# Performance work log

Hardware: AMD Instinct MI355X
Metric: run time of the kernel (lower is better)

Reference implementation:

```python
import jax, jax.numpy as jnp
import numpy as np
import math

B, LQ, LK = 4, 1024, 2048
QD, KD, VD = 768, 512, 512
H, NH = 1024, 16
HD = H // NH

def setup_inputs() -> dict:
    key = jax.random.key(0)
    ks = jax.random.split(key, 11)
    s = 0.02
    return {
        "query": jax.random.normal(ks[0], (B, LQ, QD), jnp.float32),
        "key": jax.random.normal(ks[1], (B, LK, KD), jnp.float32),
        "value": jax.random.normal(ks[2], (B, LK, VD), jnp.float32),
        "Wq": jax.random.normal(ks[3], (QD, H), jnp.float32) * s,
        "bq": jnp.zeros((H,), jnp.float32),
        "Wk": jax.random.normal(ks[4], (KD, H), jnp.float32) * s,
        "bk": jnp.zeros((H,), jnp.float32),
        "Wv": jax.random.normal(ks[5], (VD, H), jnp.float32) * s,
        "bv": jnp.zeros((H,), jnp.float32),
        "Wo": jax.random.normal(ks[6], (H, H), jnp.float32) * s,
        "bo": jnp.zeros((H,), jnp.float32),
    }

def reference(query, key, value, Wq, bq, Wk, bk, Wv, bv, Wo, bo):
    # project and split heads: [B, L, H] -> [B, NH, L, HD]
    def heads(x):
        b, l, _ = x.shape
        return x.reshape(b, l, NH, HD).transpose(0, 2, 1, 3)
    q = heads(query @ Wq + bq)   # [B, NH, LQ, HD]
    k = heads(key @ Wk + bk)     # [B, NH, LK, HD]
    v = heads(value @ Wv + bv)   # [B, NH, LK, HD]
    scores = jnp.einsum('bhqd,bhkd->bhqk', q, k) / math.sqrt(HD)
    weights = jax.nn.softmax(scores, axis=-1)  # dropout inactive (eval / rate used deterministically as identity)
    att = jnp.einsum('bhqk,bhkd->bhqd', weights, v)
    att = att.transpose(0, 2, 1, 3).reshape(query.shape[0], -1, H)
    out = att @ Wo + bo
    return out
```

## Files before the change

### kernel.cpp

```cpp
#include <hip/hip_runtime.h>
#include <math.h>

using bf16x8 = __attribute__((ext_vector_type(8))) short;
using f32x4  = __attribute__((ext_vector_type(4))) float;
using u32x2  = __attribute__((ext_vector_type(2))) unsigned int;

namespace {
constexpr int kB  = 4;
constexpr int kLQ = 1024;
constexpr int kLK = 2048;
constexpr int kH  = 1024;
constexpr int kHD = 64;
}

__device__ __forceinline__ unsigned short f2bf(float x) {
  union { float f; unsigned int u; } v; v.f = x;
  unsigned int r = v.u + 0x7fffu + ((v.u >> 16) & 1u);
  return (unsigned short)(r >> 16);
}

typedef const __attribute__((address_space(1))) unsigned int guint_t;
typedef __attribute__((address_space(3))) unsigned int luint_t;
__device__ __forceinline__ void g2l16(const void* g, void* l) {
  __builtin_amdgcn_global_load_lds(
      (guint_t*)g,
      (luint_t*)(unsigned int)(unsigned long long)l,
      16, 0, 0);
}

__global__ __launch_bounds__(256) void prep_kernel(
    const float* __restrict__ q, const float* __restrict__ k,
    const float* __restrict__ v, const float* __restrict__ Wq,
    const float* __restrict__ Wk, const float* __restrict__ Wv,
    const float* __restrict__ Wo, unsigned short* __restrict__ qo,
    unsigned short* __restrict__ ko, unsigned short* __restrict__ vo,
    unsigned short* __restrict__ WqT, unsigned short* __restrict__ WkT,
    unsigned short* __restrict__ WvT, unsigned short* __restrict__ WoT)
{
  __shared__ float tile[64][65];
  const int t = threadIdx.x;
  if (blockIdx.x < 5632) {
    int c = blockIdx.x * 256 + t;
    const float* src; unsigned short* dst;
    if (c < 393216)      { src = q; dst = qo; }
    else if (c < 917504) { src = k; dst = ko; c -= 393216; }
    else                 { src = v; dst = vo; c -= 917504; }
    const int i = c * 8;
    const float4 a = *(const float4*)(src + i);
    const float4 b = *(const float4*)(src + i + 4);
    uint4 o;
    o.x = (unsigned int)f2bf(a.x) | ((unsigned int)f2bf(a.y) << 16);
    o.y = (unsigned int)f2bf(a.z) | ((unsigned int)f2bf(a.w) << 16);
    o.z = (unsigned int)f2bf(b.x) | ((unsigned int)f2bf(b.y) << 16);
    o.w = (unsigned int)f2bf(b.z) | ((unsigned int)f2bf(b.w) << 16);
    *(uint4*)(dst + i) = o;
    return;
  }
  int id = blockIdx.x - 5632;
  const float* W; unsigned short* Wt; int Kd;
  if (id < 192)      { W = Wq; Wt = WqT; Kd = 768; }
  else if (id < 320) { W = Wk; Wt = WkT; Kd = 512;  id -= 192; }
  else if (id < 448) { W = Wv; Wt = WvT; Kd = 512;  id -= 320; }
  else               { W = Wo; Wt = WoT; Kd = 1024; id -= 448; }
  const int Nd = 1024;
  const int n0 = (id & 15) * 64;
  const int k0 = (id >> 4) * 64;
  const int rr = t >> 4;
  const int c4 = t & 15;
#pragma unroll
  for (int i = 0; i < 4; ++i) {
    const int row = i * 16 + rr;
    const float4 vv = *(const float4*)(W + (size_t)(k0 + row) * Nd + n0 + c4 * 4);
    tile[row][c4*4+0] = vv.x; tile[row][c4*4+1] = vv.y;
    tile[row][c4*4+2] = vv.z; tile[row][c4*4+3] = vv.w;
  }
  __syncthreads();
#pragma unroll
  for (int i = 0; i < 4; ++i) {
    const int n = i * 16 + rr;
    ushort4 o;
    o.x = f2bf(tile[c4*4+0][n]); o.y = f2bf(tile[c4*4+1][n]);
    o.z = f2bf(tile[c4*4+2][n]); o.w = f2bf(tile[c4*4+3][n]);
    *(ushort4*)(Wt + (size_t)(n0 + n) * Kd + k0 + c4 * 4) = o;
  }
}

__device__ __forceinline__ void gemm_body(
    const unsigned short* __restrict__ A, const unsigned short* __restrict__ Bt,
    const float* __restrict__ bias, void* __restrict__ Cout,
    int N, int K, int bx, int by, int mode, float scale, char* lds)
{
  const int t    = threadIdx.x;
  const int lane = t & 63;
  const int w    = t >> 6;
  const int l15  = lane & 15;
  const int lq8  = (lane >> 4) * 8;
  const int lq4  = (lane >> 4) * 4;
  const int r0   = by * 128;
  const int c0   = bx * 128;
  const int wm   = w >> 1, wn = w & 1;

  f32x4 acc[4][4] = {};

  const unsigned short* gsrc[4];
  char* ldst[4];
#pragma unroll
  for (int i = 0; i < 4; ++i) {
    const int g = w * 4 + i;
    const unsigned short* src = (g < 8) ? A : Bt;
    const int rbase = (g < 8) ? (r0 + g * 16) : (c0 + (g - 8) * 16);
    gsrc[i] = src + (size_t)(rbase + l15) * K + lq8;
    ldst[i] = lds + g * 1024 + lane * 16;
  }

#pragma unroll
  for (int i = 0; i < 4; ++i) g2l16(gsrc[i], ldst[i]);
#pragma unroll
  for (int i = 0; i < 4; ++i) g2l16(gsrc[i] + 32, ldst[i] + 16384);

  int slot = 0;
  for (int k0 = 0; k0 < K; k0 += 32) {
    if (k0 + 32 < K) {
      asm volatile("s_waitcnt vmcnt(4)\n\ts_barrier" ::: "memory");
    } else {
      asm volatile("s_waitcnt vmcnt(0)\n\ts_barrier" ::: "memory");
    }
    char* buf = lds + slot * 16384;
    if (k0 + 64 < K) {
      int ns = slot + 2; if (ns >= 3) ns -= 3;
#pragma unroll
      for (int i = 0; i < 4; ++i)
        g2l16(gsrc[i] + k0 + 64, ldst[i] + ns * 16384);
    }
    bf16x8 af[4], bfr[4];
#pragma unroll
    for (int i = 0; i < 4; ++i) af[i]  = *(const bf16x8*)(buf + (wm*4 + i) * 1024 + lane * 16);
#pragma unroll
    for (int j = 0; j < 4; ++j) bfr[j] = *(const bf16x8*)(buf + 8192 + (wn*4 + j) * 1024 + lane * 16);
#pragma unroll
    for (int i = 0; i < 4; ++i)
#pragma unroll
      for (int j = 0; j < 4; ++j)
        acc[i][j] = (mode == 2)
          ? __builtin_amdgcn_mfma_f32_16x16x32_bf16(af[i], bfr[j], acc[i][j], 0, 0, 0)
          : __builtin_amdgcn_mfma_f32_16x16x32_bf16(bfr[j], af[i], acc[i][j], 0, 0, 0);
    slot = (slot == 2) ? 0 : slot + 1;
  }

  if (mode == 2) {
#pragma unroll
    for (int j = 0; j < 4; ++j) {
      const int col = c0 + wn * 64 + j * 16 + l15;
      const float bcol = bias[col];
#pragma unroll
      for (int i = 0; i < 4; ++i) {
        const int row = r0 + wm * 64 + i * 16 + lq4;
        unsigned short* out = (unsigned short*)Cout;
        const int bb = row >> 11;
        const int lk = row & 2047;
        ushort4 o;
        o.x = f2bf(acc[i][j][0] + bcol); o.y = f2bf(acc[i][j][1] + bcol);
        o.z = f2bf(acc[i][j][2] + bcol); o.w = f2bf(acc[i][j][3] + bcol);
        *(ushort4*)(out + (size_t)(bb * kH + col) * kLK + lk) = o;
      }
    }
  } else {
#pragma unroll
    for (int i = 0; i < 4; ++i) {
      const int row = r0 + wm * 64 + i * 16 + l15;
#pragma unroll
      for (int j = 0; j < 4; ++j) {
        const int ncol = c0 + wn * 64 + j * 16 + lq4;
        const float4 b4 = *(const float4*)(bias + ncol);
        if (mode == 0) {
          float4 o;
          o.x = acc[i][j][0] + b4.x; o.y = acc[i][j][1] + b4.y;
          o.z = acc[i][j][2] + b4.z; o.w = acc[i][j][3] + b4.w;
          *(float4*)((float*)Cout + (size_t)row * N + ncol) = o;
        } else {
          ushort4 o;
          o.x = f2bf((acc[i][j][0] + b4.x) * scale);
          o.y = f2bf((acc[i][j][1] + b4.y) * scale);
          o.z = f2bf((acc[i][j][2] + b4.z) * scale);
          o.w = f2bf((acc[i][j][3] + b4.w) * scale);
          *(ushort4*)((unsigned short*)Cout + (size_t)row * N + ncol) = o;
        }
      }
    }
  }
}

__global__ __launch_bounds__(256) void qkv_gemm_kernel(
    const unsigned short* __restrict__ qA, const unsigned short* __restrict__ WqT,
    const float* __restrict__ bq, unsigned short* __restrict__ Qb,
    const unsigned short* __restrict__ kA, const unsigned short* __restrict__ WkT,
    const float* __restrict__ bk, unsigned short* __restrict__ Kb,
    const unsigned short* __restrict__ vA, const unsigned short* __restrict__ WvT,
    const float* __restrict__ bv, unsigned short* __restrict__ Vtw)
{
  __shared__ __align__(16) char lds[49152];
  int id = blockIdx.x;
  if (id < 256) {
    gemm_body(qA, WqT, bq, Qb, 1024, 768, id & 7, id >> 3, 1,
              0.18033688011112042f, lds);
  } else if (id < 768) {
    id -= 256;
    gemm_body(kA, WkT, bk, Kb, 1024, 512, id & 7, id >> 3, 1, 1.f, lds);
  } else {
    id -= 768;
    gemm_body(vA, WvT, bv, Vtw, 1024, 512, id & 7, id >> 3, 2, 1.f, lds);
  }
}

__global__ __launch_bounds__(256) void out_gemm_kernel(
    const unsigned short* __restrict__ A, const unsigned short* __restrict__ Bt,
    const float* __restrict__ bias, float* __restrict__ C)
{
  __shared__ __align__(16) char lds[49152];
  const int id = blockIdx.x;
  gemm_body(A, Bt, bias, C, 1024, 1024, id & 7, id >> 3, 0, 1.f, lds);
}

__global__ __launch_bounds__(512) void attn_mfma_kernel(
    const unsigned short* __restrict__ Q, const unsigned short* __restrict__ K,
    const unsigned short* __restrict__ Vt, unsigned short* __restrict__ O)
{
  __shared__ __align__(16) char lds[49152];
  constexpr int POFF = 32768;
  const int t    = threadIdx.x;
  const int lane = t & 63;
  const int w    = t >> 6;
  const int l15  = lane & 15;
  const int lg   = lane >> 4;
  const int lq8  = lg * 8;
  const int lq4  = lg * 4;
  const int flat = blockIdx.x;
  const int bh   = flat & 63;
  const int qb   = flat >> 6;
  const int h    = bh & 15;
  const int b    = bh >> 4;
  const int q0   = qb * 128;
  const int hoff = h * kHD;
  constexpr int NT = kLK / 64;

  bf16x8 qf[2];
#pragma unroll
  for (int kh = 0; kh < 2; ++kh)
    qf[kh] = *(const bf16x8*)(Q + (size_t)(b*kLQ + q0 + w*16 + l15) * kH
                                + hoff + kh*32 + lq8);

  f32x4 acc[4] = {};
  float lsum = 0.f;

  const int swz  = ((l15 * 5) & 7) << 4;
  const int colw = (lg * 8)  ^ swz;
  const int colr = (lg * 16) ^ swz;
  char* const prow = lds + POFF + (w*16 + l15) * 128;

  const unsigned short* gsrc[2];
  int gstep[2];
  char* ldst[2];
#pragma unroll
  for (int i = 0; i < 2; ++i) {
    const int g = w * 2 + i;
    if (g < 8) {
      gsrc[i]  = K + (size_t)(b*kLK + (g >> 1)*16 + l15) * kH + hoff + (g & 1)*32 + lq8;
      gstep[i] = 64 * kH;
    } else {
      const int gg = g - 8;
      gsrc[i]  = Vt + (size_t)(b*kH + hoff + (gg >> 1)*16 + l15) * kLK + (gg & 1)*32 + lq8;
      gstep[i] = 64;
    }
    ldst[i] = lds + g * 1024 + lane * 16;
  }

  g2l16(gsrc[0], ldst[0]);
  g2l16(gsrc[1], ldst[1]);

  for (int kt = 0; kt < NT; ++kt) {
    asm volatile("s_waitcnt vmcnt(0)\n\ts_barrier" ::: "memory");
    char* buf = lds + (kt & 1) * 16384;
    if (kt + 1 < NT) {
      const int ns = (kt + 1) & 1;
      g2l16(gsrc[0] + (size_t)(kt + 1) * gstep[0], ldst[0] + ns * 16384);
      g2l16(gsrc[1] + (size_t)(kt + 1) * gstep[1], ldst[1] + ns * 16384);
    }

    f32x4 s[4];
#pragma unroll
    for (int kcf = 0; kcf < 4; ++kcf) {
      const bf16x8 kf0 = *(const bf16x8*)(buf + (kcf*2 + 0) * 1024 + lane * 16);
      const bf16x8 kf1 = *(const bf16x8*)(buf + (kcf*2 + 1) * 1024 + lane * 16);
      f32x4 z = {};
      z = __builtin_amdgcn_mfma_f32_16x16x32_bf16(kf0, qf[0], z, 0, 0, 0);
      z = __builtin_amdgcn_mfma_f32_16x16x32_bf16(kf1, qf[1], z, 0, 0, 0);
      s[kcf] = z;
    }

#pragma unroll
    for (int kcf = 0; kcf < 4; ++kcf) {
      const float p0 = __builtin_amdgcn_exp2f(s[kcf][0]);
      const float p1 = __builtin_amdgcn_exp2f(s[kcf][1]);
      const float p2 = __builtin_amdgcn_exp2f(s[kcf][2]);
      const float p3 = __builtin_amdgcn_exp2f(s[kcf][3]);
      lsum += (p0 + p1) + (p2 + p3);
      u32x2 pw;
      pw.x = __builtin_amdgcn_perm(__float_as_uint(p1), __float_as_uint(p0), 0x07060302u);
      pw.y = __builtin_amdgcn_perm(__float_as_uint(p3), __float_as_uint(p2), 0x07060302u);
      *(u32x2*)(prow + (colw ^ (kcf * 32))) = pw;
    }

    bf16x8 pf[2];
#pragma unroll
    for (int kq = 0; kq < 2; ++kq)
      pf[kq] = *(const bf16x8*)(prow + (colr ^ (kq * 64)));
#pragma unroll
    for (int vd = 0; vd < 4; ++vd) {
      const bf16x8 vf0 = *(const bf16x8*)(buf + 8192 + (vd*2 + 0) * 1024 + lane * 16);
      const bf16x8 vf1 = *(const bf16x8*)(buf + 8192 + (vd*2 + 1) * 1024 + lane * 16);
      acc[vd] = __builtin_amdgcn_mfma_f32_16x16x32_bf16(vf0, pf[0], acc[vd], 0, 0, 0);
      acc[vd] = __builtin_amdgcn_mfma_f32_16x16x32_bf16(vf1, pf[1], acc[vd], 0, 0, 0);
    }
  }

  float v = lsum;
  v += __shfl_xor(v, 16);
  v += __shfl_xor(v, 32);
  const float rinv = 1.f / v;
#pragma unroll
  for (int vd = 0; vd < 4; ++vd) {
    ushort4 o;
    o.x = f2bf(acc[vd][0] * rinv);
    o.y = f2bf(acc[vd][1] * rinv);
    o.z = f2bf(acc[vd][2] * rinv);
    o.w = f2bf(acc[vd][3] * rinv);
    *(ushort4*)(O + (size_t)(b*kLQ + q0 + w*16 + l15) * kH
                  + hoff + vd*16 + lq4) = o;
  }
}

extern "C" void kernel_launch(void* const* d_in, const int* in_sizes, int n_in,
                              void* d_out, int out_size, void* d_ws, size_t ws_size,
                              hipStream_t stream) {
  (void)in_sizes; (void)n_in; (void)out_size; (void)ws_size;
  const float* query = (const float*)d_in[0];
  const float* key   = (const float*)d_in[1];
  const float* value = (const float*)d_in[2];
  const float* Wq = (const float*)d_in[3];
  const float* bq = (const float*)d_in[4];
  const float* Wk = (const float*)d_in[5];
  const float* bk = (const float*)d_in[6];
  const float* Wv = (const float*)d_in[7];
  const float* bv = (const float*)d_in[8];
  const float* Wo = (const float*)d_in[9];
  const float* bo = (const float*)d_in[10];
  float* out = (float*)d_out;

  unsigned short* ws  = (unsigned short*)d_ws;
  unsigned short* qA  = ws;
  unsigned short* kA  = qA  + 3145728;
  unsigned short* vA  = kA  + 4194304;
  unsigned short* WqT = vA  + 4194304;
  unsigned short* WkT = WqT + 786432;
  unsigned short* WvT = WkT + 524288;
  unsigned short* WoT = WvT + 524288;
  unsigned short* Qb  = WoT + 1048576;
  unsigned short* Kb  = Qb  + 4194304;
  unsigned short* Vtw = Kb  + 8388608;
  unsigned short* Ab  = Vtw + 8388608;

  prep_kernel<<<6336, 256, 0, stream>>>(query, key, value, Wq, Wk, Wv, Wo,
                                        qA, kA, vA, WqT, WkT, WvT, WoT);
  qkv_gemm_kernel<<<1280, 256, 0, stream>>>(qA, WqT, bq, Qb,
                                            kA, WkT, bk, Kb,
                                            vA, WvT, bv, Vtw);
  attn_mfma_kernel<<<512, 512, 0, stream>>>(Qb, Kb, Vtw, Ab);
  out_gemm_kernel<<<256, 256, 0, stream>>>(Ab, WoT, bo, out);
}
```

Before: 225.4 us.

## Load GEMM B operand directly from global into registers, stage only A in LDS

The projection GEMMs now stage only the A tile in LDS through the triple-buffered async path. Each wave loads its B fragments straight from global memory into registers and prefetches the next k-step's fragments during the MFMAs. LDS usage per block drops by half, which could raise occupancy and cut LDS traffic. The cost is that B is no longer shared through LDS, so global loads for B are duplicated across the two wm waves. The vmcnt waits are also retuned to account for the register loads, and B-load latency may not be fully hidden.

```diff
diff --git a/kernel.cpp b/kernel.cpp
--- a/kernel.cpp
+++ b/kernel.cpp
@@ -102,48 +102,58 @@
 
   f32x4 acc[4][4] = {};
 
-  const unsigned short* gsrc[4];
-  char* ldst[4];
-#pragma unroll
-  for (int i = 0; i < 4; ++i) {
-    const int g = w * 4 + i;
-    const unsigned short* src = (g < 8) ? A : Bt;
-    const int rbase = (g < 8) ? (r0 + g * 16) : (c0 + (g - 8) * 16);
-    gsrc[i] = src + (size_t)(rbase + l15) * K + lq8;
-    ldst[i] = lds + g * 1024 + lane * 16;
-  }
-
-#pragma unroll
-  for (int i = 0; i < 4; ++i) g2l16(gsrc[i], ldst[i]);
-#pragma unroll
-  for (int i = 0; i < 4; ++i) g2l16(gsrc[i] + 32, ldst[i] + 16384);
+  const unsigned short* gsrcA[2];
+  char* ldstA[2];
+#pragma unroll
+  for (int i = 0; i < 2; ++i) {
+    const int g = w * 2 + i;
+    gsrcA[i] = A + (size_t)(r0 + g * 16 + l15) * K + lq8;
+    ldstA[i] = lds + g * 1024 + lane * 16;
+  }
+  const unsigned short* gB[4];
+#pragma unroll
+  for (int j = 0; j < 4; ++j)
+    gB[j] = Bt + (size_t)(c0 + (wn*4 + j) * 16 + l15) * K + lq8;
+
+  g2l16(gsrcA[0], ldstA[0]);
+  g2l16(gsrcA[1], ldstA[1]);
+  asm volatile("" ::: "memory");
+  bf16x8 bcur[4], bnxt[4];
+#pragma unroll
+  for (int j = 0; j < 4; ++j) bcur[j] = *(const bf16x8*)(gB[j]);
+  asm volatile("" ::: "memory");
+  g2l16(gsrcA[0] + 32, ldstA[0] + 8192);
+  g2l16(gsrcA[1] + 32, ldstA[1] + 8192);
 
   int slot = 0;
   for (int k0 = 0; k0 < K; k0 += 32) {
     if (k0 + 32 < K) {
+      asm volatile("s_waitcnt vmcnt(6)\n\ts_barrier" ::: "memory");
+    } else {
       asm volatile("s_waitcnt vmcnt(4)\n\ts_barrier" ::: "memory");
-    } else {
-      asm volatile("s_waitcnt vmcnt(0)\n\ts_barrier" ::: "memory");
-    }
-    char* buf = lds + slot * 16384;
+    }
+    char* buf = lds + slot * 8192;
     if (k0 + 64 < K) {
       int ns = slot + 2; if (ns >= 3) ns -= 3;
-#pragma unroll
-      for (int i = 0; i < 4; ++i)
-        g2l16(gsrc[i] + k0 + 64, ldst[i] + ns * 16384);
-    }
-    bf16x8 af[4], bfr[4];
-#pragma unroll
-    for (int i = 0; i < 4; ++i) af[i]  = *(const bf16x8*)(buf + (wm*4 + i) * 1024 + lane * 16);
-#pragma unroll
-    for (int j = 0; j < 4; ++j) bfr[j] = *(const bf16x8*)(buf + 8192 + (wn*4 + j) * 1024 + lane * 16);
+      g2l16(gsrcA[0] + k0 + 64, ldstA[0] + ns * 8192);
+      g2l16(gsrcA[1] + k0 + 64, ldstA[1] + ns * 8192);
+    }
+    bf16x8 af[4];
+#pragma unroll
+    for (int i = 0; i < 4; ++i) af[i] = *(const bf16x8*)(buf + (wm*4 + i) * 1024 + lane * 16);
 #pragma unroll
     for (int i = 0; i < 4; ++i)
 #pragma unroll
       for (int j = 0; j < 4; ++j)
         acc[i][j] = (mode == 2)
-          ? __builtin_amdgcn_mfma_f32_16x16x32_bf16(af[i], bfr[j], acc[i][j], 0, 0, 0)
-          : __builtin_amdgcn_mfma_f32_16x16x32_bf16(bfr[j], af[i], acc[i][j], 0, 0, 0);
+          ? __builtin_amdgcn_mfma_f32_16x16x32_bf16(af[i], bcur[j], acc[i][j], 0, 0, 0)
+          : __builtin_amdgcn_mfma_f32_16x16x32_bf16(bcur[j], af[i], acc[i][j], 0, 0, 0);
+    if (k0 + 32 < K) {
+#pragma unroll
+      for (int j = 0; j < 4; ++j) bnxt[j] = *(const bf16x8*)(gB[j] + k0 + 32);
+#pragma unroll
+      for (int j = 0; j < 4; ++j) bcur[j] = bnxt[j];
+    }
     slot = (slot == 2) ? 0 : slot + 1;
   }
 
@@ -198,7 +208,7 @@
     const unsigned short* __restrict__ vA, const unsigned short* __restrict__ WvT,
     const float* __restrict__ bv, unsigned short* __restrict__ Vtw)
 {
-  __shared__ __align__(16) char lds[49152];
+  __shared__ __align__(16) char lds[24576];
   int id = blockIdx.x;
   if (id < 256) {
     gemm_body(qA, WqT, bq, Qb, 1024, 768, id & 7, id >> 3, 1,
@@ -216,7 +226,7 @@
     const unsigned short* __restrict__ A, const unsigned short* __restrict__ Bt,
     const float* __restrict__ bias, float* __restrict__ C)
 {
-  __shared__ __align__(16) char lds[49152];
+  __shared__ __align__(16) char lds[24576];
   const int id = blockIdx.x;
   gemm_body(A, Bt, bias, C, 1024, 1024, id & 7, id >> 3, 0, 1.f, lds);
 }
```

Measured after the change: 274.3 us. +21.7%, slower.

## Rewrite output projection GEMM with 512 threads and triple-buffered async LDS loads

Applied to the files above, without the earlier changes.

Replaces the generic gemm_body call for the output projection with a dedicated kernel using 8 waves per 128x128 tile. Each wave holds a 32x64 sub-tile and loads K-slices directly into LDS through global_load_lds, using a three-slot ring with one barrier per step. The aim is more waves per tile to hide latency, and better overlap of global loads with MFMA work, in the small 256-block output GEMM. The cost is a fragment layout specialised to this one GEMM, and per-step barriers across more waves.

```diff
diff --git a/kernel.cpp b/kernel.cpp
--- a/kernel.cpp
+++ b/kernel.cpp
@@ -212,13 +212,81 @@
   }
 }
 
-__global__ __launch_bounds__(256) void out_gemm_kernel(
+__global__ __launch_bounds__(512) void out_gemm_kernel(
     const unsigned short* __restrict__ A, const unsigned short* __restrict__ Bt,
     const float* __restrict__ bias, float* __restrict__ C)
 {
   __shared__ __align__(16) char lds[49152];
-  const int id = blockIdx.x;
-  gemm_body(A, Bt, bias, C, 1024, 1024, id & 7, id >> 3, 0, 1.f, lds);
+  const int id   = blockIdx.x;
+  const int t    = threadIdx.x;
+  const int lane = t & 63;
+  const int w    = t >> 6;
+  const int l15  = lane & 15;
+  const int lq8  = (lane >> 4) * 8;
+  const int lq4  = (lane >> 4) * 4;
+  const int r0   = (id >> 3) * 128;
+  const int c0   = (id & 7) * 128;
+  const int wm   = w >> 1;
+  const int wn   = w & 1;
+  constexpr int K = 1024, N = 1024;
+
+  f32x4 acc[2][4] = {};
+
+  const unsigned short* gsrc[2];
+  char* ldst[2];
+#pragma unroll
+  for (int i = 0; i < 2; ++i) {
+    const int g = w * 2 + i;
+    const unsigned short* src = (g < 8) ? A : Bt;
+    const int rbase = (g < 8) ? (r0 + g * 16) : (c0 + (g - 8) * 16);
+    gsrc[i] = src + (size_t)(rbase + l15) * K + lq8;
+    ldst[i] = lds + g * 1024 + lane * 16;
+  }
+
+  g2l16(gsrc[0], ldst[0]);
+  g2l16(gsrc[1], ldst[1]);
+  g2l16(gsrc[0] + 32, ldst[0] + 16384);
+  g2l16(gsrc[1] + 32, ldst[1] + 16384);
+
+  int slot = 0;
+  for (int k0 = 0; k0 < K; k0 += 32) {
+    if (k0 + 32 < K) {
+      asm volatile("s_waitcnt vmcnt(2)\n\ts_barrier" ::: "memory");
+    } else {
+      asm volatile("s_waitcnt vmcnt(0)\n\ts_barrier" ::: "memory");
+    }
+    char* buf = lds + slot * 16384;
+    if (k0 + 64 < K) {
+      int ns = slot + 2; if (ns >= 3) ns -= 3;
+      g2l16(gsrc[0] + k0 + 64, ldst[0] + ns * 16384);
+      g2l16(gsrc[1] + k0 + 64, ldst[1] + ns * 16384);
+    }
+    bf16x8 af[2], bfr[4];
+#pragma unroll
+    for (int i = 0; i < 2; ++i) af[i]  = *(const bf16x8*)(buf + (wm*2 + i) * 1024 + lane * 16);
+#pragma unroll
+    for (int j = 0; j < 4; ++j) bfr[j] = *(const bf16x8*)(buf + 8192 + (wn*4 + j) * 1024 + lane * 16);
+#pragma unroll
+    for (int i = 0; i < 2; ++i)
+#pragma unroll
+      for (int j = 0; j < 4; ++j)
+        acc[i][j] = __builtin_amdgcn_mfma_f32_16x16x32_bf16(bfr[j], af[i], acc[i][j], 0, 0, 0);
+    slot = (slot == 2) ? 0 : slot + 1;
+  }
+
+#pragma unroll
+  for (int i = 0; i < 2; ++i) {
+    const int row = r0 + wm * 32 + i * 16 + l15;
+#pragma unroll
+    for (int j = 0; j < 4; ++j) {
+      const int ncol = c0 + wn * 64 + j * 16 + lq4;
+      const float4 b4 = *(const float4*)(bias + ncol);
+      float4 o;
+      o.x = acc[i][j][0] + b4.x; o.y = acc[i][j][1] + b4.y;
+      o.z = acc[i][j][2] + b4.z; o.w = acc[i][j][3] + b4.w;
+      *(float4*)(C + (size_t)row * N + ncol) = o;
+    }
+  }
 }
 
 __global__ __launch_bounds__(512) void attn_mfma_kernel(
@@ -375,5 +443,5 @@
                                             kA, WkT, bk, Kb,
                                             vA, WvT, bv, Vtw);
   attn_mfma_kernel<<<512, 512, 0, stream>>>(Qb, Kb, Vtw, Ab);
-  out_gemm_kernel<<<256, 256, 0, stream>>>(Ab, WoT, bo, out);
-}
+  out_gemm_kernel<<<256, 512, 0, stream>>>(Ab, WoT, bo, out);
+}
```

Result: no change. 226.7 us (+0.5%).

## Widen GEMM tiles to 128x256 and switch to double-buffered LDS pipeline

Applied to the files above, without the earlier changes.

The shared GEMM body now computes 128x256 output tiles, each wave holding a 64x128 accumulator, which halves the block counts of the QKV and output-projection launches. Each loaded A fragment is reused across more columns. The three-stage LDS ring with a partial vmcnt wait is replaced by a two-slot double buffer that waits for all loads before every step. The aim is less global and LDS traffic per MFMA, at the cost of more registers, less prefetch depth and fewer blocks (128 for the output GEMM) to spread over the CUs.

```diff
diff --git a/kernel.cpp b/kernel.cpp
--- a/kernel.cpp
+++ b/kernel.cpp
@@ -97,60 +97,60 @@
   const int lq8  = (lane >> 4) * 8;
   const int lq4  = (lane >> 4) * 4;
   const int r0   = by * 128;
-  const int c0   = bx * 128;
-  const int wm   = w >> 1, wn = w & 1;
-
-  f32x4 acc[4][4] = {};
-
-  const unsigned short* gsrc[4];
-  char* ldst[4];
-#pragma unroll
-  for (int i = 0; i < 4; ++i) {
-    const int g = w * 4 + i;
-    const unsigned short* src = (g < 8) ? A : Bt;
-    const int rbase = (g < 8) ? (r0 + g * 16) : (c0 + (g - 8) * 16);
-    gsrc[i] = src + (size_t)(rbase + l15) * K + lq8;
-    ldst[i] = lds + g * 1024 + lane * 16;
-  }
-
-#pragma unroll
-  for (int i = 0; i < 4; ++i) g2l16(gsrc[i], ldst[i]);
-#pragma unroll
-  for (int i = 0; i < 4; ++i) g2l16(gsrc[i] + 32, ldst[i] + 16384);
+  const int c0   = bx * 256;
+  const int wm   = w >> 1;
+  const int wn   = w & 1;
+
+  f32x4 acc[4][8] = {};
+
+  const unsigned short* gsrc[6];
+  char* ldst[6];
+#pragma unroll
+  for (int i = 0; i < 6; ++i) {
+    const int g = w * 6 + i;
+    if (g < 8) {
+      gsrc[i] = A + (size_t)(r0 + g * 16 + l15) * K + lq8;
+      ldst[i] = lds + g * 1024 + lane * 16;
+    } else {
+      const int cg = g - 8;
+      gsrc[i] = Bt + (size_t)(c0 + cg * 16 + l15) * K + lq8;
+      ldst[i] = lds + 8192 + cg * 1024 + lane * 16;
+    }
+  }
+
+#pragma unroll
+  for (int i = 0; i < 6; ++i) g2l16(gsrc[i], ldst[i]);
 
   int slot = 0;
   for (int k0 = 0; k0 < K; k0 += 32) {
+    asm volatile("s_waitcnt vmcnt(0)\n\ts_barrier" ::: "memory");
+    char* buf = lds + slot * 24576;
     if (k0 + 32 < K) {
-      asm volatile("s_waitcnt vmcnt(4)\n\ts_barrier" ::: "memory");
-    } else {
-      asm volatile("s_waitcnt vmcnt(0)\n\ts_barrier" ::: "memory");
-    }
-    char* buf = lds + slot * 16384;
-    if (k0 + 64 < K) {
-      int ns = slot + 2; if (ns >= 3) ns -= 3;
+      const int off = (slot ^ 1) * 24576;
+#pragma unroll
+      for (int i = 0; i < 6; ++i)
+        g2l16(gsrc[i] + k0 + 32, ldst[i] + off);
+    }
+    bf16x8 af[4];
+#pragma unroll
+    for (int i = 0; i < 4; ++i)
+      af[i] = *(const bf16x8*)(buf + (wm*4 + i) * 1024 + lane * 16);
+#pragma unroll
+    for (int j = 0; j < 8; ++j) {
+      const bf16x8 bf = *(const bf16x8*)(buf + 8192 + (wn*8 + j) * 1024 + lane * 16);
 #pragma unroll
       for (int i = 0; i < 4; ++i)
-        g2l16(gsrc[i] + k0 + 64, ldst[i] + ns * 16384);
-    }
-    bf16x8 af[4], bfr[4];
-#pragma unroll
-    for (int i = 0; i < 4; ++i) af[i]  = *(const bf16x8*)(buf + (wm*4 + i) * 1024 + lane * 16);
-#pragma unroll
-    for (int j = 0; j < 4; ++j) bfr[j] = *(const bf16x8*)(buf + 8192 + (wn*4 + j) * 1024 + lane * 16);
-#pragma unroll
-    for (int i = 0; i < 4; ++i)
-#pragma unroll
-      for (int j = 0; j < 4; ++j)
         acc[i][j] = (mode == 2)
-          ? __builtin_amdgcn_mfma_f32_16x16x32_bf16(af[i], bfr[j], acc[i][j], 0, 0, 0)
-          : __builtin_amdgcn_mfma_f32_16x16x32_bf16(bfr[j], af[i], acc[i][j], 0, 0, 0);
-    slot = (slot == 2) ? 0 : slot + 1;
+          ? __builtin_amdgcn_mfma_f32_16x16x32_bf16(af[i], bf, acc[i][j], 0, 0, 0)
+          : __builtin_amdgcn_mfma_f32_16x16x32_bf16(bf, af[i], acc[i][j], 0, 0, 0);
+    }
+    slot ^= 1;
   }
 
   if (mode == 2) {
 #pragma unroll
-    for (int j = 0; j < 4; ++j) {
-      const int col = c0 + wn * 64 + j * 16 + l15;
+    for (int j = 0; j < 8; ++j) {
+      const int col = c0 + wn * 128 + j * 16 + l15;
       const float bcol = bias[col];
 #pragma unroll
       for (int i = 0; i < 4; ++i) {
@@ -169,8 +169,8 @@
     for (int i = 0; i < 4; ++i) {
       const int row = r0 + wm * 64 + i * 16 + l15;
 #pragma unroll
-      for (int j = 0; j < 4; ++j) {
-        const int ncol = c0 + wn * 64 + j * 16 + lq4;
+      for (int j = 0; j < 8; ++j) {
+        const int ncol = c0 + wn * 128 + j * 16 + lq4;
         const float4 b4 = *(const float4*)(bias + ncol);
         if (mode == 0) {
           float4 o;
@@ -200,15 +200,15 @@
 {
   __shared__ __align__(16) char lds[49152];
   int id = blockIdx.x;
-  if (id < 256) {
-    gemm_body(qA, WqT, bq, Qb, 1024, 768, id & 7, id >> 3, 1,
+  if (id < 128) {
+    gemm_body(qA, WqT, bq, Qb, 1024, 768, id & 3, id >> 2, 1,
               0.18033688011112042f, lds);
-  } else if (id < 768) {
-    id -= 256;
-    gemm_body(kA, WkT, bk, Kb, 1024, 512, id & 7, id >> 3, 1, 1.f, lds);
+  } else if (id < 384) {
+    id -= 128;
+    gemm_body(kA, WkT, bk, Kb, 1024, 512, id & 3, id >> 2, 1, 1.f, lds);
   } else {
-    id -= 768;
-    gemm_body(vA, WvT, bv, Vtw, 1024, 512, id & 7, id >> 3, 2, 1.f, lds);
+    id -= 384;
+    gemm_body(vA, WvT, bv, Vtw, 1024, 512, id & 3, id >> 2, 2, 1.f, lds);
   }
 }
 
@@ -218,7 +218,7 @@
 {
   __shared__ __align__(16) char lds[49152];
   const int id = blockIdx.x;
-  gemm_body(A, Bt, bias, C, 1024, 1024, id & 7, id >> 3, 0, 1.f, lds);
+  gemm_body(A, Bt, bias, C, 1024, 1024, id & 3, id >> 2, 0, 1.f, lds);
 }
 
 __global__ __launch_bounds__(512) void attn_mfma_kernel(
@@ -371,9 +371,9 @@
 
   prep_kernel<<<6336, 256, 0, stream>>>(query, key, value, Wq, Wk, Wv, Wo,
                                         qA, kA, vA, WqT, WkT, WvT, WoT);
-  qkv_gemm_kernel<<<1280, 256, 0, stream>>>(qA, WqT, bq, Qb,
-                                            kA, WkT, bk, Kb,
-                                            vA, WvT, bv, Vtw);
+  qkv_gemm_kernel<<<640, 256, 0, stream>>>(qA, WqT, bq, Qb,
+                                           kA, WkT, bk, Kb,
+                                           vA, WvT, bv, Vtw);
   attn_mfma_kernel<<<512, 512, 0, stream>>>(Qb, Kb, Vtw, Ab);
-  out_gemm_kernel<<<256, 256, 0, stream>>>(Ab, WoT, bo, out);
-}
+  out_gemm_kernel<<<128, 256, 0, stream>>>(Ab, WoT, bo, out);
+}
```

Measured after the change: 247.6 us. +9.8%, slower.
